# Optimization experiments

Measured on AMD Instinct MI355X. Metric: run time of the kernel, lower is better.

Reference implementation:

```python
import jax, jax.numpy as jnp
import numpy as np

N, S, B, E = 32768, 1024, 32, 262144   # nodes, nodes-per-graph, graphs, edges
C, H, L = 128, 4, 4                    # hidden, heads, layers
ND, ED, PE = 64, 16, 16                # node_dim, edge_dim, pe_dim
DH = C // H
LN_EPS = 1e-5


def _mlp2(h, w1, b1, w2, b2, act=jax.nn.relu):
    # mlp(ch_in, ch_out, hidden, num_hidden_layers=1): Linear -> act -> Linear (dropout = identity at inference)
    return act(h @ w1 + b1) @ w2 + b2


def _layer_norm(h, g, b):
    mu = jnp.mean(h, axis=-1, keepdims=True)
    var = jnp.var(h, axis=-1, keepdims=True)
    return (h - mu) * jax.lax.rsqrt(var + LN_EPS) * g + b


def setup_inputs() -> dict:
    key = jax.random.key(0)
    ks = iter(jax.random.split(key, 64))
    def nrm(shape, scale=0.05):
        return jax.random.normal(next(ks), shape, jnp.float32) * scale
    x = jax.random.normal(next(ks), (N, ND), jnp.float32)
    lap_pe = jax.random.normal(next(ks), (N, PE), jnp.float32)
    edge_attr = jax.random.normal(next(ks), (E, ED), jnp.float32)
    # edges within graphs: each graph occupies a contiguous block of S nodes
    g = jax.random.randint(next(ks), (E,), 0, B)
    src = g * S + jax.random.randint(next(ks), (E,), 0, S)
    dst = g * S + jax.random.randint(next(ks), (E,), 0, S)
    edge_index = jnp.stack([src, dst]).astype(jnp.int32)
    batch = (jnp.arange(N) // S).astype(jnp.int32)
    inp = dict(x=x, edge_index=edge_index, batch=batch, edge_attr=edge_attr, lap_pe=lap_pe)
    inp.update(
        node_w1=nrm((ND + PE, C)), node_b1=jnp.zeros((C,)), node_w2=nrm((C, C)), node_b2=jnp.zeros((C,)),
        edge_w1=nrm((ED, C)), edge_b1=jnp.zeros((C,)), edge_w2=nrm((C, C)), edge_b2=jnp.zeros((C,)),
        eps=jnp.zeros((L,)),
        gin_w1=nrm((L, C, C)), gin_b1=jnp.zeros((L, C)), gin_w2=nrm((L, C, C)), gin_b2=jnp.zeros((L, C)),
        elin_w=nrm((L, C, C)), elin_b=jnp.zeros((L, C)),
        attn_qkv_w=nrm((L, C, 3 * C)), attn_qkv_b=jnp.zeros((L, 3 * C)),
        attn_out_w=nrm((L, C, C)), attn_out_b=jnp.zeros((L, C)),
        mlp_w1=nrm((L, C, 2 * C)), mlp_b1=jnp.zeros((L, 2 * C)),
        mlp_w2=nrm((L, 2 * C, C)), mlp_b2=jnp.zeros((L, C)),
        ln1_g=jnp.ones((L, C)), ln1_b=jnp.zeros((L, C)),
        ln2_g=jnp.ones((L, C)), ln2_b=jnp.zeros((L, C)),
        ln3_g=jnp.ones((L, C)), ln3_b=jnp.zeros((L, C)),
        post_w1=nrm((C, C)), post_b1=jnp.zeros((C,)), post_w2=nrm((C, C)), post_b2=jnp.zeros((C,)),
        ro_w1=nrm((C, C)), ro_b1=jnp.zeros((C,)), ro_w2=nrm((C, 1)), ro_b2=jnp.zeros((1,)),
    )
    return inp


def reference(x, edge_index, batch, edge_attr, lap_pe,
              node_w1, node_b1, node_w2, node_b2,
              edge_w1, edge_b1, edge_w2, edge_b2,
              eps, gin_w1, gin_b1, gin_w2, gin_b2, elin_w, elin_b,
              attn_qkv_w, attn_qkv_b, attn_out_w, attn_out_b,
              mlp_w1, mlp_b1, mlp_w2, mlp_b2,
              ln1_g, ln1_b, ln2_g, ln2_b, ln3_g, ln3_b,
              post_w1, post_b1, post_w2, post_b2,
              ro_w1, ro_b1, ro_w2, ro_b2):
    src, dst = edge_index[0], edge_index[1]
    x = jnp.concatenate([x, lap_pe], axis=-1)
    x = _mlp2(x, node_w1, node_b1, node_w2, node_b2)
    e = _mlp2(edge_attr, edge_w1, edge_b1, edge_w2, edge_b2)
    scale = 1.0 / np.sqrt(DH)
    for i in range(L):
        # --- local GINEConv: nn((1+eps)*x_i + sum_j relu(x_j + lin(e_ij))) ---
        m = jax.nn.relu(x[src] + e @ elin_w[i] + elin_b[i])           # [E, C]
        agg = jax.ops.segment_sum(m, dst, num_segments=N)             # [N, C]
        hl = _mlp2((1.0 + eps[i]) * x + agg, gin_w1[i], gin_b1[i], gin_w2[i], gin_b2[i])
        hl = _layer_norm(hl + x, ln1_g[i], ln1_b[i])
        # --- global multihead attention over dense per-graph batch (equal sizes => reshape) ---
        xd = x.reshape(B, S, C)
        q, k, v = jnp.split(xd @ attn_qkv_w[i] + attn_qkv_b[i], 3, axis=-1)
        q = q.reshape(B, S, H, DH).transpose(0, 2, 1, 3)              # [B,H,S,DH]
        k = k.reshape(B, S, H, DH).transpose(0, 2, 1, 3)
        v = v.reshape(B, S, H, DH).transpose(0, 2, 1, 3)
        att = jax.nn.softmax(jnp.einsum('bhqd,bhkd->bhqk', q, k) * scale, axis=-1)
        o = jnp.einsum('bhqk,bhkd->bhqd', att, v).transpose(0, 2, 1, 3).reshape(B, S, C)
        ha = (o @ attn_out_w[i] + attn_out_b[i]).reshape(N, C)
        ha = _layer_norm(ha + x, ln2_g[i], ln2_b[i])
        # --- combine + FFN (act='gelu') + norm3, then outer residual ---
        out = hl + ha
        out = out + _mlp2(out, mlp_w1[i], mlp_b1[i], mlp_w2[i], mlp_b2[i], act=jax.nn.gelu)
        h = _layer_norm(out, ln3_g[i], ln3_b[i])
        x = x + h
    x = x + _mlp2(x, post_w1, post_b1, post_w2, post_b2)
    sums = jax.ops.segment_sum(x, batch, num_segments=B)
    cnt = jax.ops.segment_sum(jnp.ones((N, 1), x.dtype), batch, num_segments=B)
    gmean = sums / cnt
    return _mlp2(gmean, ro_w1, ro_b1, ro_w2, ro_b2)                   # [B, 1]
```

## Files before the change

### kernel.cpp

```cpp
#include <hip/hip_runtime.h>
#include <math.h>

namespace {

constexpr int N_  = 32768;
constexpr int S_  = 1024;
constexpr int B_  = 32;
constexpr int E_  = 262144;
constexpr int C_  = 128;
constexpr int ND_ = 64;
constexpr int PE_ = 16;
constexpr int ED_ = 16;
constexpr float LNE = 1e-5f;

typedef __attribute__((ext_vector_type(8))) short short8;
typedef __attribute__((ext_vector_type(4))) float floatx4;

__device__ inline float gelu_tanh(float v) {
  const float c = 0.7978845608028654f;
  return 0.5f * v * (1.0f + tanhf(c * (v + 0.044715f * v * v * v)));
}

__device__ inline unsigned short f2bf_u(float f) {
  unsigned u = __float_as_uint(f);
  u += 0x7fff + ((u >> 16) & 1);
  return (unsigned short)(u >> 16);
}

__device__ inline float bf2f(unsigned short v) {
  return __uint_as_float(((unsigned)v) << 16);
}

__device__ inline float block_sum128(float v, float* red, int t) {
  red[t] = v;
  __syncthreads();
#pragma unroll
  for (int off = 64; off > 0; off >>= 1) {
    if (t < off) red[t] += red[t + off];
    __syncthreads();
  }
  float r = red[0];
  __syncthreads();
  return r;
}

__global__ void k_zero(float4* __restrict__ p, int n4) {
  int i = blockIdx.x * 256 + threadIdx.x;
  if (i < n4) p[i] = make_float4(0.f, 0.f, 0.f, 0.f);
}

__global__ void k_count(const int* __restrict__ dst, int* __restrict__ hist) {
  int e = blockIdx.x * 256 + threadIdx.x;
  if (e < E_) atomicAdd(&hist[dst[e]], 1);
}

__global__ __launch_bounds__(1024) void k_scan(int* __restrict__ hist, int* __restrict__ binStart) {
  __shared__ int sums[1024];
  int t = threadIdx.x;
  int base = t * 32;
  int loc[32];
  int s = 0;
#pragma unroll
  for (int i = 0; i < 32; ++i) { loc[i] = s; s += hist[base + i]; }
  sums[t] = s;
  __syncthreads();
  for (int off = 1; off < 1024; off <<= 1) {
    int v = (t >= off) ? sums[t - off] : 0;
    __syncthreads();
    sums[t] += v;
    __syncthreads();
  }
  int excl = sums[t] - s;
#pragma unroll
  for (int i = 0; i < 32; ++i) {
    int v = excl + loc[i];
    binStart[base + i] = v;
    hist[base + i] = v;
  }
  if (t == 1023) binStart[32768] = sums[1023];
}

__global__ void k_scatter(const int* __restrict__ dst, int* __restrict__ cursor,
                          int* __restrict__ perm) {
  int e = blockIdx.x * 256 + threadIdx.x;
  if (e < E_) {
    int p = atomicAdd(&cursor[dst[e]], 1);
    perm[p] = e;
  }
}

__global__ void k_gather_edges(const float* __restrict__ ea, const int* __restrict__ src,
                               const int* __restrict__ dst, const int* __restrict__ perm,
                               float* __restrict__ ea_s, int* __restrict__ src_s,
                               int* __restrict__ dst_s) {
  int p4 = blockIdx.x * 256 + threadIdx.x;
  int p = p4 >> 2, c4 = p4 & 3;
  int e = perm[p];
  ((float4*)(ea_s + (size_t)p * ED_))[c4] = ((const float4*)(ea + (size_t)e * ED_))[c4];
  if (c4 == 0) { src_s[p] = src[e]; dst_s[p] = dst[e]; }
}

__global__ void k_fuse_w(const float* __restrict__ w2, const float* __restrict__ b2,
                         const float* __restrict__ elin_w, const float* __restrict__ elin_b,
                         unsigned short* __restrict__ fw2t, float* __restrict__ fb2) {
  int t = threadIdx.x;
  int bid = blockIdx.x;
  int layer = bid / (C_ + 1);
  int k = bid % (C_ + 1);
  const float* el = elin_w + (size_t)layer * C_ * C_;
  if (k < C_) {
    float a = 0.0f;
    for (int m = 0; m < C_; ++m) a += w2[k * C_ + m] * el[m * C_ + t];
    fw2t[(size_t)layer * C_ * C_ + t * C_ + k] = f2bf_u(a);
  } else {
    float a = elin_b[layer * C_ + t];
    for (int m = 0; m < C_; ++m) a += b2[m] * el[m * C_ + t];
    fb2[layer * C_ + t] = a;
  }
}

__global__ void k_prep_ew1(const float* __restrict__ ew1, unsigned short* __restrict__ ew1t) {
  int n = blockIdx.x;
  int k = threadIdx.x;
  ew1t[n * 32 + k] = (k < ED_) ? f2bf_u(ew1[k * C_ + n]) : (unsigned short)0;
}

__global__ void k_prep(const float* __restrict__ gin_w1, const float* __restrict__ gin_w2,
                       const float* __restrict__ aqkv_w, const float* __restrict__ aout_w,
                       const float* __restrict__ mlp_w1, const float* __restrict__ mlp_w2,
                       unsigned short* __restrict__ wt) {
  int t = threadIdx.x;
  int bid = blockIdx.x;
  int l = bid / 1152;
  int r = bid % 1152;
  unsigned short* base = wt + (size_t)l * 163840;
  if (r < 128) {
    base[r * 128 + t] = f2bf_u(gin_w1[(size_t)l * 16384 + t * 128 + r]);
  } else if (r < 256) {
    int n = r - 128;
    base[16384 + n * 128 + t] = f2bf_u(gin_w2[(size_t)l * 16384 + t * 128 + n]);
  } else if (r < 640) {
    int n = r - 256;
    base[32768 + n * 128 + t] = f2bf_u(aqkv_w[(size_t)l * 49152 + t * 384 + n]);
  } else if (r < 768) {
    int n = r - 640;
    base[81920 + n * 128 + t] = f2bf_u(aout_w[(size_t)l * 16384 + t * 128 + n]);
  } else if (r < 1024) {
    int n = r - 768;
    base[98304 + n * 128 + t] = f2bf_u(mlp_w1[(size_t)l * 32768 + t * 256 + n]);
  } else {
    int n = r - 1024;
    base[131072 + n * 256 + t]       = f2bf_u(mlp_w2[(size_t)l * 32768 + t * 128 + n]);
    base[131072 + n * 256 + 128 + t] = f2bf_u(mlp_w2[(size_t)l * 32768 + (t + 128) * 128 + n]);
  }
}

__global__ void k_node_enc(const float* __restrict__ xin, const float* __restrict__ pe,
                           const float* __restrict__ w1, const float* __restrict__ b1,
                           const float* __restrict__ w2, const float* __restrict__ b2,
                           float* __restrict__ xout) {
  __shared__ float inL[4][80];
  __shared__ float hidL[4][C_];
  int t = threadIdx.x;
  int row0 = blockIdx.x * 4;
#pragma unroll
  for (int r = 0; r < 4; ++r) {
    int row = row0 + r;
    if (t < ND_) inL[r][t] = xin[(size_t)row * ND_ + t];
    else if (t < 80) inL[r][t] = pe[(size_t)row * PE_ + (t - ND_)];
  }
  __syncthreads();
  float acc[4];
  float bb = b1[t];
#pragma unroll
  for (int r = 0; r < 4; ++r) acc[r] = bb;
  for (int k = 0; k < 80; ++k) {
    float wv = w1[k * C_ + t];
#pragma unroll
    for (int r = 0; r < 4; ++r) acc[r] += inL[r][k] * wv;
  }
#pragma unroll
  for (int r = 0; r < 4; ++r) hidL[r][t] = fmaxf(acc[r], 0.0f);
  __syncthreads();
  float bb2 = b2[t];
#pragma unroll
  for (int r = 0; r < 4; ++r) acc[r] = bb2;
  for (int k = 0; k < C_; ++k) {
    float wv = w2[k * C_ + t];
#pragma unroll
    for (int r = 0; r < 4; ++r) acc[r] += hidL[r][k] * wv;
  }
#pragma unroll
  for (int r = 0; r < 4; ++r) xout[(size_t)(row0 + r) * C_ + t] = acc[r];
}

__global__ __launch_bounds__(256) void k_edge_mfma(
    const float* __restrict__ ea_s, const float* __restrict__ x,
    const int* __restrict__ src_s, const int* __restrict__ dst_s,
    const unsigned short* __restrict__ ew1t, const float* __restrict__ eb1,
    const unsigned short* __restrict__ fw2t, const float* __restrict__ fb2,
    float* __restrict__ agg) {
  __shared__ unsigned short eaL[64][40];
  __shared__ unsigned short buf[64][136];
  __shared__ int srcL[64], dstL[64];
  int tid = threadIdx.x;
  int e0 = blockIdx.x * 64;

  if (tid < 64) { srcL[tid] = src_s[e0 + tid]; dstL[tid] = dst_s[e0 + tid]; }
  {
    int r = tid >> 2, c4 = tid & 3;
    float4 v = ((const float4*)(ea_s + (size_t)(e0 + r) * ED_))[c4];
    ushort4 u;
    u.x = f2bf_u(v.x); u.y = f2bf_u(v.y); u.z = f2bf_u(v.z); u.w = f2bf_u(v.w);
    *(ushort4*)&eaL[r][c4 * 4] = u;
    ushort4 z4 = {0, 0, 0, 0};
    *(ushort4*)&eaL[r][16 + c4 * 4] = z4;
  }
  __syncthreads();

  int lane = tid & 63;
  int w = tid >> 6;
  int li = lane & 15;
  int quad = lane >> 4;
  int r0 = w * 16;

  short8 aE = *(const short8*)&eaL[r0 + li][quad * 8];
#pragma unroll
  for (int t8 = 0; t8 < 8; ++t8) {
    short8 bE = *(const short8*)(ew1t + (size_t)(t8 * 16 + li) * 32 + quad * 8);
    floatx4 z = {0.f, 0.f, 0.f, 0.f};
    floatx4 h = __builtin_amdgcn_mfma_f32_16x16x32_bf16(aE, bE, z, 0, 0, 0);
    float bv = eb1[t8 * 16 + li];
#pragma unroll
    for (int reg = 0; reg < 4; ++reg)
      buf[r0 + quad * 4 + reg][t8 * 16 + li] = f2bf_u(fmaxf(h[reg] + bv, 0.f));
  }
  __syncthreads();

  short8 aK[4];
#pragma unroll
  for (int k4 = 0; k4 < 4; ++k4)
    aK[k4] = *(const short8*)&buf[r0 + li][k4 * 32 + quad * 8];
  __syncthreads();

  float fbv[8];
#pragma unroll
  for (int t8 = 0; t8 < 8; ++t8) fbv[t8] = fb2[t8 * 16 + li];

#pragma unroll
  for (int t8 = 0; t8 < 8; ++t8) {
    floatx4 acc = {0.f, 0.f, 0.f, 0.f};
    const unsigned short* bp = fw2t + (size_t)(t8 * 16 + li) * C_ + quad * 8;
#pragma unroll
    for (int k4 = 0; k4 < 4; ++k4) {
      short8 bf = *(const short8*)(bp + k4 * 32);
      acc = __builtin_amdgcn_mfma_f32_16x16x32_bf16(aK[k4], bf, acc, 0, 0, 0);
    }
    int n = t8 * 16 + li;
#pragma unroll
    for (int reg = 0; reg < 4; ++reg) {
      int cr = r0 + quad * 4 + reg;
      float v = fmaxf(acc[reg] + fbv[t8] + x[(size_t)srcL[cr] * C_ + n], 0.0f);
      buf[cr][n] = f2bf_u(v);
    }
  }
  __syncthreads();

  {
    int col = tid & 127;
    int rbase = (tid >> 7) * 32;
    float run = bf2f(buf[rbase][col]);
    int cur = dstL[rbase];
    for (int r = 1; r < 32; ++r) {
      int rr = rbase + r;
      int d = dstL[rr];
      float v = bf2f(buf[rr][col]);
      if (d != cur) {
        atomicAdd(&agg[(size_t)cur * C_ + col], run);
        run = v; cur = d;
      } else {
        run += v;
      }
    }
    atomicAdd(&agg[(size_t)cur * C_ + col], run);
  }
}

__global__ __launch_bounds__(256) void k_ginqkv(
    const float* __restrict__ x, const float* __restrict__ agg,
    const unsigned short* __restrict__ w1t, const float* __restrict__ b1,
    const unsigned short* __restrict__ w2t, const float* __restrict__ b2,
    const float* __restrict__ g, const float* __restrict__ bln,
    const float* __restrict__ epsarr, int layer, float* __restrict__ hl,
    const unsigned short* __restrict__ qkvt, const float* __restrict__ qb,
    unsigned short* __restrict__ qkvb) {
  __shared__ unsigned short inL[64][136];
  __shared__ unsigned short xbL[64][136];
  int tid = threadIdx.x;
  int row0 = blockIdx.x * 64;
  float epsv = 1.0f + epsarr[layer];
#pragma unroll
  for (int i = 0; i < 8; ++i) {
    int p = i * 256 + tid;
    int r = p >> 5, c4 = p & 31;
    float4 xa = *(const float4*)(x + (size_t)(row0 + r) * C_ + c4 * 4);
    float4 ag = *(const float4*)(agg + (size_t)(row0 + r) * C_ + c4 * 4);
    ushort4 ux;
    ux.x = f2bf_u(xa.x); ux.y = f2bf_u(xa.y); ux.z = f2bf_u(xa.z); ux.w = f2bf_u(xa.w);
    *(ushort4*)&xbL[r][c4 * 4] = ux;
    ushort4 u;
    u.x = f2bf_u(epsv * xa.x + ag.x);
    u.y = f2bf_u(epsv * xa.y + ag.y);
    u.z = f2bf_u(epsv * xa.z + ag.z);
    u.w = f2bf_u(epsv * xa.w + ag.w);
    *(ushort4*)&inL[r][c4 * 4] = u;
  }
  __syncthreads();
  int lane = tid & 63, w = tid >> 6, li = lane & 15, quad = lane >> 4;
  int r0 = w * 16;

  short8 aK[4];
#pragma unroll
  for (int k4 = 0; k4 < 4; ++k4) aK[k4] = *(const short8*)&inL[r0 + li][k4 * 32 + quad * 8];
#pragma unroll
  for (int t8 = 0; t8 < 8; ++t8) {
    floatx4 acc = {0.f, 0.f, 0.f, 0.f};
    const unsigned short* bp = w1t + (size_t)(t8 * 16 + li) * 128 + quad * 8;
#pragma unroll
    for (int k4 = 0; k4 < 4; ++k4) {
      short8 bf = *(const short8*)(bp + k4 * 32);
      acc = __builtin_amdgcn_mfma_f32_16x16x32_bf16(aK[k4], bf, acc, 0, 0, 0);
    }
    float bv = b1[t8 * 16 + li];
#pragma unroll
    for (int reg = 0; reg < 4; ++reg)
      inL[r0 + quad * 4 + reg][t8 * 16 + li] = f2bf_u(fmaxf(acc[reg] + bv, 0.f));
  }
  short8 aK2[4];
#pragma unroll
  for (int k4 = 0; k4 < 4; ++k4) aK2[k4] = *(const short8*)&inL[r0 + li][k4 * 32 + quad * 8];
  floatx4 acc2[8];
#pragma unroll
  for (int t8 = 0; t8 < 8; ++t8) acc2[t8] = (floatx4){0.f, 0.f, 0.f, 0.f};
#pragma unroll
  for (int t8 = 0; t8 < 8; ++t8) {
    const unsigned short* bp = w2t + (size_t)(t8 * 16 + li) * 128 + quad * 8;
#pragma unroll
    for (int k4 = 0; k4 < 4; ++k4) {
      short8 bf = *(const short8*)(bp + k4 * 32);
      acc2[t8] = __builtin_amdgcn_mfma_f32_16x16x32_bf16(aK2[k4], bf, acc2[t8], 0, 0, 0);
    }
  }
  float gv[8], blv[8], b2v[8];
#pragma unroll
  for (int t8 = 0; t8 < 8; ++t8) {
    int col = t8 * 16 + li;
    gv[t8] = g[col]; blv[t8] = bln[col]; b2v[t8] = b2[col];
  }
#pragma unroll
  for (int reg = 0; reg < 4; ++reg) {
    int row = row0 + r0 + quad * 4 + reg;
    float v[8], s = 0.f, s2 = 0.f;
#pragma unroll
    for (int t8 = 0; t8 < 8; ++t8) {
      float xv = x[(size_t)row * C_ + t8 * 16 + li];
      v[t8] = acc2[t8][reg] + b2v[t8] + xv;
      s += v[t8]; s2 += v[t8] * v[t8];
    }
#pragma unroll
    for (int m = 1; m <= 8; m <<= 1) { s += __shfl_xor(s, m); s2 += __shfl_xor(s2, m); }
    float mu = s * (1.0f / C_);
    float var = s2 * (1.0f / C_) - mu * mu;
    float inv = rsqrtf(var + LNE);
#pragma unroll
    for (int t8 = 0; t8 < 8; ++t8)
      hl[(size_t)row * C_ + t8 * 16 + li] = (v[t8] - mu) * inv * gv[t8] + blv[t8];
  }

  short8 aQ[4];
#pragma unroll
  for (int k4 = 0; k4 < 4; ++k4) aQ[k4] = *(const short8*)&xbL[r0 + li][k4 * 32 + quad * 8];
#pragma unroll
  for (int t8 = 0; t8 < 24; ++t8) {
    floatx4 acc = {0.f, 0.f, 0.f, 0.f};
    const unsigned short* bp = qkvt + (size_t)(t8 * 16 + li) * 128 + quad * 8;
#pragma unroll
    for (int k4 = 0; k4 < 4; ++k4) {
      short8 bf = *(const short8*)(bp + k4 * 32);
      acc = __builtin_amdgcn_mfma_f32_16x16x32_bf16(aQ[k4], bf, acc, 0, 0, 0);
    }
    int col = t8 * 16 + li;
    float bv = qb[col];
#pragma unroll
    for (int reg = 0; reg < 4; ++reg) {
      int row = row0 + r0 + quad * 4 + reg;
      qkvb[(size_t)row * 384 + col] = f2bf_u(acc[reg] + bv);
    }
  }
}

__global__ __launch_bounds__(256) void k_attn_mfma(const unsigned short* __restrict__ qkvb,
                                                   float* __restrict__ attno) {
  __shared__ unsigned short kL[2][32][40];
  __shared__ unsigned short vT[2][32][40];
  __shared__ unsigned short pL[4][16][40];
  int tid = threadIdx.x;
  int lane = tid & 63;
  int w = tid >> 6;
  int li = lane & 15;
  int quad = lane >> 4;
  int bid = blockIdx.x;
  int b = (bid & 7) * 4 + ((bid >> 3) & 3);
  int rest = bid >> 5;
  int h = rest & 3;
  int qt = rest >> 2;
  int qbase = b * S_ + qt * 64 + w * 16;

  short8 qA = *(const short8*)(qkvb + (size_t)(qbase + li) * 384 + h * 32 + quad * 8);

  floatx4 o0 = {0.f, 0.f, 0.f, 0.f}, o1 = {0.f, 0.f, 0.f, 0.f};
  float lsum[4] = {0.f, 0.f, 0.f, 0.f};
  const float scale = 0.17677669529663687f;

  int half = tid >> 7;
  int tt = tid & 127;
  int j = tt >> 2;
  int seg = tt & 3;
  int vcol = (((j >> 3) ^ seg) & 3) * 8 + (j & 7);
  int vg0 = ((quad ^ (li >> 3)) & 3) * 8;
  int vg1 = ((quad ^ (2 + (li >> 3))) & 3) * 8;

  const unsigned short* pbase = qkvb + (half ? 256 : 128) + h * 32 + seg * 8;

  short8 val = *(const short8*)(pbase + (size_t)(b * S_ + 0 * 32 + j) * 384);

  for (int kc = 0; kc < 32; ++kc) {
    int buf = kc & 1;
    if (half == 0) {
      *(short8*)&kL[buf][j][seg * 8] = val;
    } else {
#pragma unroll
      for (int i = 0; i < 8; ++i) vT[buf][seg * 8 + i][vcol] = (unsigned short)val[i];
    }
    __syncthreads();
    if (kc < 31)
      val = *(const short8*)(pbase + (size_t)(b * S_ + (kc + 1) * 32 + j) * 384);
    short8 kB0 = *(const short8*)&kL[buf][li][quad * 8];
    short8 kB1 = *(const short8*)&kL[buf][16 + li][quad * 8];
    floatx4 z = {0.f, 0.f, 0.f, 0.f};
    floatx4 s0 = __builtin_amdgcn_mfma_f32_16x16x32_bf16(qA, kB0, z, 0, 0, 0);
    floatx4 s1 = __builtin_amdgcn_mfma_f32_16x16x32_bf16(qA, kB1, z, 0, 0, 0);
#pragma unroll
    for (int r = 0; r < 4; ++r) {
      float p0 = __expf(s0[r] * scale);
      float p1 = __expf(s1[r] * scale);
      lsum[r] += p0 + p1;
      pL[w][quad * 4 + r][li] = f2bf_u(p0);
      pL[w][quad * 4 + r][16 + li] = f2bf_u(p1);
    }
    short8 pA  = *(const short8*)&pL[w][li][quad * 8];
    short8 vB0 = *(const short8*)&vT[buf][li][vg0];
    short8 vB1 = *(const short8*)&vT[buf][16 + li][vg1];
    o0 = __builtin_amdgcn_mfma_f32_16x16x32_bf16(pA, vB0, o0, 0, 0, 0);
    o1 = __builtin_amdgcn_mfma_f32_16x16x32_bf16(pA, vB1, o1, 0, 0, 0);
  }
#pragma unroll
  for (int r = 0; r < 4; ++r) {
    float l = lsum[r];
#pragma unroll
    for (int msk = 1; msk <= 8; msk <<= 1) l += __shfl_xor(l, msk);
    float inv = 1.0f / l;
    size_t row = (size_t)(qbase + quad * 4 + r);
    attno[row * C_ + h * 32 + li] = o0[r] * inv;
    attno[row * C_ + h * 32 + 16 + li] = o1[r] * inv;
  }
}

__global__ __launch_bounds__(256) void k_aoffn(
    const float* __restrict__ attno, float* __restrict__ x,
    const float* __restrict__ hl,
    const unsigned short* __restrict__ aot, const float* __restrict__ ab,
    const float* __restrict__ g2, const float* __restrict__ bl2,
    const unsigned short* __restrict__ w1t, const float* __restrict__ b1,
    const unsigned short* __restrict__ w2t, const float* __restrict__ b2,
    const float* __restrict__ g3, const float* __restrict__ bl3) {
  __shared__ unsigned short inL[64][136];
  __shared__ unsigned short hidL[64][264];
  int tid = threadIdx.x;
  int row0 = blockIdx.x * 64;
#pragma unroll
  for (int i = 0; i < 8; ++i) {
    int p = i * 256 + tid;
    int r = p >> 5, c4 = p & 31;
    float4 xa = *(const float4*)(attno + (size_t)(row0 + r) * C_ + c4 * 4);
    ushort4 u;
    u.x = f2bf_u(xa.x); u.y = f2bf_u(xa.y); u.z = f2bf_u(xa.z); u.w = f2bf_u(xa.w);
    *(ushort4*)&inL[r][c4 * 4] = u;
  }
  __syncthreads();
  int lane = tid & 63, w = tid >> 6, li = lane & 15, quad = lane >> 4;
  int r0 = w * 16;

  short8 aK[4];
#pragma unroll
  for (int k4 = 0; k4 < 4; ++k4) aK[k4] = *(const short8*)&inL[r0 + li][k4 * 32 + quad * 8];
  floatx4 acc[8];
#pragma unroll
  for (int t8 = 0; t8 < 8; ++t8) acc[t8] = (floatx4){0.f, 0.f, 0.f, 0.f};
#pragma unroll
  for (int t8 = 0; t8 < 8; ++t8) {
    const unsigned short* bp = aot + (size_t)(t8 * 16 + li) * 128 + quad * 8;
#pragma unroll
    for (int k4 = 0; k4 < 4; ++k4) {
      short8 bf = *(const short8*)(bp + k4 * 32);
      acc[t8] = __builtin_amdgcn_mfma_f32_16x16x32_bf16(aK[k4], bf, acc[t8], 0, 0, 0);
    }
  }
  float g2v[8], bl2v[8], abv[8];
#pragma unroll
  for (int t8 = 0; t8 < 8; ++t8) {
    int col = t8 * 16 + li;
    g2v[t8] = g2[col]; bl2v[t8] = bl2[col]; abv[t8] = ab[col];
  }
  float outv[8][4];
#pragma unroll
  for (int reg = 0; reg < 4; ++reg) {
    int row = row0 + r0 + quad * 4 + reg;
    float v[8], s = 0.f, s2 = 0.f;
#pragma unroll
    for (int t8 = 0; t8 < 8; ++t8) {
      float xv = x[(size_t)row * C_ + t8 * 16 + li];
      v[t8] = acc[t8][reg] + abv[t8] + xv;
      s += v[t8]; s2 += v[t8] * v[t8];
    }
#pragma unroll
    for (int m = 1; m <= 8; m <<= 1) { s += __shfl_xor(s, m); s2 += __shfl_xor(s2, m); }
    float mu = s * (1.0f / C_);
    float var = s2 * (1.0f / C_) - mu * mu;
    float inv = rsqrtf(var + LNE);
#pragma unroll
    for (int t8 = 0; t8 < 8; ++t8) {
      int col = t8 * 16 + li;
      float ha = (v[t8] - mu) * inv * g2v[t8] + bl2v[t8];
      float ov = hl[(size_t)row * C_ + col] + ha;
      outv[t8][reg] = ov;
      inL[r0 + quad * 4 + reg][col] = f2bf_u(ov);
    }
  }

  short8 aK2[4];
#pragma unroll
  for (int k4 = 0; k4 < 4; ++k4) aK2[k4] = *(const short8*)&inL[r0 + li][k4 * 32 + quad * 8];
#pragma unroll
  for (int t8 = 0; t8 < 16; ++t8) {
    floatx4 a1 = {0.f, 0.f, 0.f, 0.f};
    const unsigned short* bp = w1t + (size_t)(t8 * 16 + li) * 128 + quad * 8;
#pragma unroll
    for (int k4 = 0; k4 < 4; ++k4) {
      short8 bf = *(const short8*)(bp + k4 * 32);
      a1 = __builtin_amdgcn_mfma_f32_16x16x32_bf16(aK2[k4], bf, a1, 0, 0, 0);
    }
    float bv = b1[t8 * 16 + li];
#pragma unroll
    for (int reg = 0; reg < 4; ++reg)
      hidL[r0 + quad * 4 + reg][t8 * 16 + li] = f2bf_u(gelu_tanh(a1[reg] + bv));
  }
  short8 aK3[8];
#pragma unroll
  for (int k4 = 0; k4 < 8; ++k4) aK3[k4] = *(const short8*)&hidL[r0 + li][k4 * 32 + quad * 8];
  floatx4 acc2[8];
#pragma unroll
  for (int t8 = 0; t8 < 8; ++t8) acc2[t8] = (floatx4){0.f, 0.f, 0.f, 0.f};
#pragma unroll
  for (int t8 = 0; t8 < 8; ++t8) {
    const unsigned short* bp = w2t + (size_t)(t8 * 16 + li) * 256 + quad * 8;
#pragma unroll
    for (int k4 = 0; k4 < 8; ++k4) {
      short8 bf = *(const short8*)(bp + k4 * 32);
      acc2[t8] = __builtin_amdgcn_mfma_f32_16x16x32_bf16(aK3[k4], bf, acc2[t8], 0, 0, 0);
    }
  }
  float g3v[8], bl3v[8], b2v[8];
#pragma unroll
  for (int t8 = 0; t8 < 8; ++t8) {
    int col = t8 * 16 + li;
    g3v[t8] = g3[col]; bl3v[t8] = bl3[col]; b2v[t8] = b2[col];
  }
#pragma unroll
  for (int reg = 0; reg < 4; ++reg) {
    int row = row0 + r0 + quad * 4 + reg;
    float v[8], s = 0.f, s2 = 0.f;
#pragma unroll
    for (int t8 = 0; t8 < 8; ++t8) {
      v[t8] = acc2[t8][reg] + b2v[t8] + outv[t8][reg];
      s += v[t8]; s2 += v[t8] * v[t8];
    }
#pragma unroll
    for (int m = 1; m <= 8; m <<= 1) { s += __shfl_xor(s, m); s2 += __shfl_xor(s2, m); }
    float mu = s * (1.0f / C_);
    float var = s2 * (1.0f / C_) - mu * mu;
    float inv = rsqrtf(var + LNE);
#pragma unroll
    for (int t8 = 0; t8 < 8; ++t8) {
      size_t idx = (size_t)row * C_ + t8 * 16 + li;
      x[idx] = x[idx] + (v[t8] - mu) * inv * g3v[t8] + bl3v[t8];
    }
  }
}

__global__ void k_post(float* __restrict__ x,
                       const float* __restrict__ w1, const float* __restrict__ b1,
                       const float* __restrict__ w2, const float* __restrict__ b2) {
  __shared__ float inL[4][C_];
  __shared__ float hidL[4][C_];
  int t = threadIdx.x;
  int row0 = blockIdx.x * 4;
  float xv[4];
#pragma unroll
  for (int r = 0; r < 4; ++r) {
    size_t idx = (size_t)(row0 + r) * C_ + t;
    xv[r] = x[idx];
    inL[r][t] = xv[r];
  }
  __syncthreads();
  float acc[4];
  float bb = b1[t];
#pragma unroll
  for (int r = 0; r < 4; ++r) acc[r] = bb;
  for (int k = 0; k < C_; ++k) {
    float wv = w1[k * C_ + t];
#pragma unroll
    for (int r = 0; r < 4; ++r) acc[r] += inL[r][k] * wv;
  }
#pragma unroll
  for (int r = 0; r < 4; ++r) hidL[r][t] = fmaxf(acc[r], 0.0f);
  __syncthreads();
  float bb2 = b2[t];
#pragma unroll
  for (int r = 0; r < 4; ++r) acc[r] = bb2;
  for (int k = 0; k < C_; ++k) {
    float wv = w2[k * C_ + t];
#pragma unroll
    for (int r = 0; r < 4; ++r) acc[r] += hidL[r][k] * wv;
  }
#pragma unroll
  for (int r = 0; r < 4; ++r) {
    size_t idx = (size_t)(row0 + r) * C_ + t;
    x[idx] = xv[r] + acc[r];
  }
}

__global__ void k_pool(const float* __restrict__ x, float* __restrict__ gmean) {
  int t = threadIdx.x;
  int b = blockIdx.x;
  float s = 0.0f;
  for (int sidx = 0; sidx < S_; ++sidx) s += x[((size_t)b * S_ + sidx) * C_ + t];
  gmean[b * C_ + t] = s * (1.0f / S_);
}

__global__ void k_readout(const float* __restrict__ gmean,
                          const float* __restrict__ w1, const float* __restrict__ b1,
                          const float* __restrict__ w2, const float* __restrict__ b2,
                          float* __restrict__ out) {
  __shared__ float gL[C_];
  __shared__ float red[C_];
  int t = threadIdx.x;
  int b = blockIdx.x;
  gL[t] = gmean[b * C_ + t];
  __syncthreads();
  float acc = b1[t];
  for (int k = 0; k < C_; ++k) acc += gL[k] * w1[k * C_ + t];
  float hid = fmaxf(acc, 0.0f);
  float part = hid * w2[t];
  float tot = block_sum128(part, red, t);
  if (t == 0) out[b] = tot + b2[0];
}

}

extern "C" void kernel_launch(void* const* d_in, const int* in_sizes, int n_in,
                              void* d_out, int out_size, void* d_ws, size_t ws_size,
                              hipStream_t stream) {
  const float* in_x      = (const float*)d_in[0];
  const int*   edge_idx  = (const int*)d_in[1];
  const float* edge_attr = (const float*)d_in[3];
  const float* lap_pe    = (const float*)d_in[4];
  const float* node_w1 = (const float*)d_in[5];
  const float* node_b1 = (const float*)d_in[6];
  const float* node_w2 = (const float*)d_in[7];
  const float* node_b2 = (const float*)d_in[8];
  const float* edge_w1 = (const float*)d_in[9];
  const float* edge_b1 = (const float*)d_in[10];
  const float* edge_w2 = (const float*)d_in[11];
  const float* edge_b2 = (const float*)d_in[12];
  const float* eps     = (const float*)d_in[13];
  const float* gin_w1  = (const float*)d_in[14];
  const float* gin_b1  = (const float*)d_in[15];
  const float* gin_w2  = (const float*)d_in[16];
  const float* gin_b2  = (const float*)d_in[17];
  const float* elin_w  = (const float*)d_in[18];
  const float* elin_b  = (const float*)d_in[19];
  const float* aqkv_w  = (const float*)d_in[20];
  const float* aqkv_b  = (const float*)d_in[21];
  const float* aout_w  = (const float*)d_in[22];
  const float* aout_b  = (const float*)d_in[23];
  const float* mlp_w1  = (const float*)d_in[24];
  const float* mlp_b1  = (const float*)d_in[25];
  const float* mlp_w2  = (const float*)d_in[26];
  const float* mlp_b2  = (const float*)d_in[27];
  const float* ln1_g   = (const float*)d_in[28];
  const float* ln1_b   = (const float*)d_in[29];
  const float* ln2_g   = (const float*)d_in[30];
  const float* ln2_b   = (const float*)d_in[31];
  const float* ln3_g   = (const float*)d_in[32];
  const float* ln3_b   = (const float*)d_in[33];
  const float* post_w1 = (const float*)d_in[34];
  const float* post_b1 = (const float*)d_in[35];
  const float* post_w2 = (const float*)d_in[36];
  const float* post_b2 = (const float*)d_in[37];
  const float* ro_w1   = (const float*)d_in[38];
  const float* ro_b1   = (const float*)d_in[39];
  const float* ro_w2   = (const float*)d_in[40];
  const float* ro_b2   = (const float*)d_in[41];

  const int* src = edge_idx;
  const int* dst = edge_idx + E_;

  float* ws = (float*)d_ws;
  float* x     = ws;
  unsigned short* qkvb = (unsigned short*)(x + (size_t)N_ * C_);
  float* hl    = x + (size_t)N_ * C_ + (size_t)N_ * 192;
  float* attno = hl + (size_t)N_ * C_;
  float* agg   = attno;
  float* fb2   = attno + (size_t)N_ * C_;
  unsigned short* fw2tb = (unsigned short*)(fb2 + 4 * C_);
  unsigned short* wt = fw2tb + (size_t)4 * C_ * C_;
  unsigned short* ew1tb = wt + 655360;
  float* ea_s  = (float*)(ew1tb + 4096);
  int* src_s   = (int*)(ea_s + (size_t)E_ * ED_);
  int* dst_s   = src_s + E_;
  int* hist    = dst_s + E_;
  int* binStart = hist + 32768;
  int* perm    = binStart + 32769;
  float* gmean = hl;

  float* out = (float*)d_out;

  dim3 blk(128);
  const size_t LWS = 163840;

  k_fuse_w<<<4 * (C_ + 1), blk, 0, stream>>>(edge_w2, edge_b2, elin_w, elin_b, fw2tb, fb2);
  k_prep<<<4 * 1152, blk, 0, stream>>>(gin_w1, gin_w2, aqkv_w, aout_w, mlp_w1, mlp_w2, wt);
  k_prep_ew1<<<128, 32, 0, stream>>>(edge_w1, ew1tb);
  k_zero<<<(32768 / 4 + 255) / 256, 256, 0, stream>>>((float4*)hist, 32768 / 4);
  k_count<<<E_ / 256, 256, 0, stream>>>(dst, hist);
  k_scan<<<1, 1024, 0, stream>>>(hist, binStart);
  k_scatter<<<E_ / 256, 256, 0, stream>>>(dst, hist, perm);
  k_gather_edges<<<E_ * 4 / 256, 256, 0, stream>>>(edge_attr, src, dst, perm,
                                                   ea_s, src_s, dst_s);
  k_node_enc<<<N_ / 4, blk, 0, stream>>>(in_x, lap_pe, node_w1, node_b1, node_w2, node_b2, x);

  for (int i = 0; i < 4; ++i) {
    const unsigned short* wl = wt + (size_t)i * LWS;
    k_zero<<<(N_ * C_ / 4 + 255) / 256, 256, 0, stream>>>((float4*)agg, N_ * C_ / 4);
    k_edge_mfma<<<E_ / 64, 256, 0, stream>>>(ea_s, x, src_s, dst_s,
                                             ew1tb, edge_b1,
                                             fw2tb + (size_t)i * C_ * C_, fb2 + i * C_, agg);
    k_ginqkv<<<N_ / 64, 256, 0, stream>>>(x, agg,
                                          wl + 0, gin_b1 + i * C_,
                                          wl + 16384, gin_b2 + i * C_,
                                          ln1_g + i * C_, ln1_b + i * C_, eps, i, hl,
                                          wl + 32768, aqkv_b + i * 384, qkvb);
    k_attn_mfma<<<B_ * 4 * 16, 256, 0, stream>>>(qkvb, attno);
    k_aoffn<<<N_ / 64, 256, 0, stream>>>(attno, x, hl,
                                         wl + 81920, aout_b + i * C_,
                                         ln2_g + i * C_, ln2_b + i * C_,
                                         wl + 98304, mlp_b1 + i * 256,
                                         wl + 131072, mlp_b2 + i * C_,
                                         ln3_g + i * C_, ln3_b + i * C_);
  }

  k_post<<<N_ / 4, blk, 0, stream>>>(x, post_w1, post_b1, post_w2, post_b2);
  k_pool<<<B_, blk, 0, stream>>>(x, gmean);
  k_readout<<<B_, blk, 0, stream>>>(gmean, ro_w1, ro_b1, ro_w2, ro_b2, out);
}
```

Baseline: 1.412 ms.

## Store edge attrs in bf16, prefetch source rows to LDS, fuse pooling into post MLP

The edge-gather pass now converts edge attributes to bf16 once, so the per-layer edge kernel reads half the bytes. The edge kernel prefetches the source node rows into shared memory with coalesced float4 loads before the first MFMA stage, replacing scattered per-element reads in the epilogue. It stores them as bf16, which loses some precision in the residual add. The post MLP also accumulates per-graph sums through atomics, removing the separate pooling kernel that walked 1024 rows serially per graph.

After: 1.242 ms. 12.1% less time.

```diff
diff --git a/kernel.cpp b/kernel.cpp
--- a/kernel.cpp
+++ b/kernel.cpp
@@ -91,13 +91,22 @@
 
 __global__ void k_gather_edges(const float* __restrict__ ea, const int* __restrict__ src,
                                const int* __restrict__ dst, const int* __restrict__ perm,
-                               float* __restrict__ ea_s, int* __restrict__ src_s,
+                               unsigned short* __restrict__ ea_b, int* __restrict__ src_s,
                                int* __restrict__ dst_s) {
-  int p4 = blockIdx.x * 256 + threadIdx.x;
-  int p = p4 >> 2, c4 = p4 & 3;
+  int p = blockIdx.x * 256 + threadIdx.x;
+  if (p >= E_) return;
   int e = perm[p];
-  ((float4*)(ea_s + (size_t)p * ED_))[c4] = ((const float4*)(ea + (size_t)e * ED_))[c4];
-  if (c4 == 0) { src_s[p] = src[e]; dst_s[p] = dst[e]; }
+  const float4* s = (const float4*)(ea + (size_t)e * ED_);
+  unsigned short* d = ea_b + (size_t)p * ED_;
+#pragma unroll
+  for (int i = 0; i < 4; ++i) {
+    float4 v = s[i];
+    ushort4 u;
+    u.x = f2bf_u(v.x); u.y = f2bf_u(v.y); u.z = f2bf_u(v.z); u.w = f2bf_u(v.w);
+    *(ushort4*)(d + i * 4) = u;
+  }
+  src_s[p] = src[e];
+  dst_s[p] = dst[e];
 }
 
 __global__ void k_fuse_w(const float* __restrict__ w2, const float* __restrict__ b2,
@@ -195,28 +204,36 @@
 }
 
 __global__ __launch_bounds__(256) void k_edge_mfma(
-    const float* __restrict__ ea_s, const float* __restrict__ x,
+    const unsigned short* __restrict__ ea_b, const float* __restrict__ x,
     const int* __restrict__ src_s, const int* __restrict__ dst_s,
     const unsigned short* __restrict__ ew1t, const float* __restrict__ eb1,
     const unsigned short* __restrict__ fw2t, const float* __restrict__ fb2,
     float* __restrict__ agg) {
-  __shared__ unsigned short eaL[64][40];
+  __shared__ unsigned short eaL[64][32];
   __shared__ unsigned short buf[64][136];
+  __shared__ unsigned short xrL[64][136];
   __shared__ int srcL[64], dstL[64];
   int tid = threadIdx.x;
   int e0 = blockIdx.x * 64;
 
   if (tid < 64) { srcL[tid] = src_s[e0 + tid]; dstL[tid] = dst_s[e0 + tid]; }
-  {
-    int r = tid >> 2, c4 = tid & 3;
-    float4 v = ((const float4*)(ea_s + (size_t)(e0 + r) * ED_))[c4];
-    ushort4 u;
-    u.x = f2bf_u(v.x); u.y = f2bf_u(v.y); u.z = f2bf_u(v.z); u.w = f2bf_u(v.w);
-    *(ushort4*)&eaL[r][c4 * 4] = u;
-    ushort4 z4 = {0, 0, 0, 0};
-    *(ushort4*)&eaL[r][16 + c4 * 4] = z4;
-  }
-  __syncthreads();
+  if (tid < 128) {
+    int r = tid >> 1, hf = tid & 1;
+    *(short8*)&eaL[r][hf * 8] = *(const short8*)(ea_b + (size_t)(e0 + r) * ED_ + hf * 8);
+  } else {
+    int r = (tid - 128) >> 1, hf = (tid - 128) & 1;
+    short8 z = {0, 0, 0, 0, 0, 0, 0, 0};
+    *(short8*)&eaL[r][16 + hf * 8] = z;
+  }
+  __syncthreads();
+
+  float4 xv[8];
+#pragma unroll
+  for (int it = 0; it < 8; ++it) {
+    int idx = it * 256 + tid;
+    int r = idx >> 5, c4 = idx & 31;
+    xv[it] = *(const float4*)(x + (size_t)srcL[r] * C_ + c4 * 4);
+  }
 
   int lane = tid & 63;
   int w = tid >> 6;
@@ -235,13 +252,22 @@
     for (int reg = 0; reg < 4; ++reg)
       buf[r0 + quad * 4 + reg][t8 * 16 + li] = f2bf_u(fmaxf(h[reg] + bv, 0.f));
   }
+
+#pragma unroll
+  for (int it = 0; it < 8; ++it) {
+    int idx = it * 256 + tid;
+    int r = idx >> 5, c4 = idx & 31;
+    ushort4 u;
+    u.x = f2bf_u(xv[it].x); u.y = f2bf_u(xv[it].y);
+    u.z = f2bf_u(xv[it].z); u.w = f2bf_u(xv[it].w);
+    *(ushort4*)&xrL[r][c4 * 4] = u;
+  }
   __syncthreads();
 
   short8 aK[4];
 #pragma unroll
   for (int k4 = 0; k4 < 4; ++k4)
     aK[k4] = *(const short8*)&buf[r0 + li][k4 * 32 + quad * 8];
-  __syncthreads();
 
   float fbv[8];
 #pragma unroll
@@ -260,7 +286,7 @@
 #pragma unroll
     for (int reg = 0; reg < 4; ++reg) {
       int cr = r0 + quad * 4 + reg;
-      float v = fmaxf(acc[reg] + fbv[t8] + x[(size_t)srcL[cr] * C_ + n], 0.0f);
+      float v = fmaxf(acc[reg] + fbv[t8] + bf2f(xrL[cr][n]), 0.0f);
       buf[cr][n] = f2bf_u(v);
     }
   }
@@ -608,9 +634,10 @@
   }
 }
 
-__global__ void k_post(float* __restrict__ x,
-                       const float* __restrict__ w1, const float* __restrict__ b1,
-                       const float* __restrict__ w2, const float* __restrict__ b2) {
+__global__ void k_post_pool(float* __restrict__ x,
+                            const float* __restrict__ w1, const float* __restrict__ b1,
+                            const float* __restrict__ w2, const float* __restrict__ b2,
+                            float* __restrict__ gsum) {
   __shared__ float inL[4][C_];
   __shared__ float hidL[4][C_];
   int t = threadIdx.x;
@@ -643,22 +670,19 @@
 #pragma unroll
     for (int r = 0; r < 4; ++r) acc[r] += hidL[r][k] * wv;
   }
+  float local = 0.f;
 #pragma unroll
   for (int r = 0; r < 4; ++r) {
     size_t idx = (size_t)(row0 + r) * C_ + t;
-    x[idx] = xv[r] + acc[r];
-  }
-}
-
-__global__ void k_pool(const float* __restrict__ x, float* __restrict__ gmean) {
-  int t = threadIdx.x;
-  int b = blockIdx.x;
-  float s = 0.0f;
-  for (int sidx = 0; sidx < S_; ++sidx) s += x[((size_t)b * S_ + sidx) * C_ + t];
-  gmean[b * C_ + t] = s * (1.0f / S_);
-}
-
-__global__ void k_readout(const float* __restrict__ gmean,
+    float nv = xv[r] + acc[r];
+    x[idx] = nv;
+    local += nv;
+  }
+  int b = row0 / S_;
+  atomicAdd(&gsum[b * C_ + t], local);
+}
+
+__global__ void k_readout(const float* __restrict__ gsum,
                           const float* __restrict__ w1, const float* __restrict__ b1,
                           const float* __restrict__ w2, const float* __restrict__ b2,
                           float* __restrict__ out) {
@@ -666,7 +690,7 @@
   __shared__ float red[C_];
   int t = threadIdx.x;
   int b = blockIdx.x;
-  gL[t] = gmean[b * C_ + t];
+  gL[t] = gsum[b * C_ + t] * (1.0f / S_);
   __syncthreads();
   float acc = b1[t];
   for (int k = 0; k < C_; ++k) acc += gL[k] * w1[k * C_ + t];
@@ -736,13 +760,13 @@
   unsigned short* fw2tb = (unsigned short*)(fb2 + 4 * C_);
   unsigned short* wt = fw2tb + (size_t)4 * C_ * C_;
   unsigned short* ew1tb = wt + 655360;
-  float* ea_s  = (float*)(ew1tb + 4096);
-  int* src_s   = (int*)(ea_s + (size_t)E_ * ED_);
+  unsigned short* ea_b = ew1tb + 4096;
+  int* src_s   = (int*)(ea_b + (size_t)E_ * ED_);
   int* dst_s   = src_s + E_;
   int* hist    = dst_s + E_;
   int* binStart = hist + 32768;
   int* perm    = binStart + 32769;
-  float* gmean = hl;
+  float* gsum  = hl;
 
   float* out = (float*)d_out;
 
@@ -756,14 +780,14 @@
   k_count<<<E_ / 256, 256, 0, stream>>>(dst, hist);
   k_scan<<<1, 1024, 0, stream>>>(hist, binStart);
   k_scatter<<<E_ / 256, 256, 0, stream>>>(dst, hist, perm);
-  k_gather_edges<<<E_ * 4 / 256, 256, 0, stream>>>(edge_attr, src, dst, perm,
-                                                   ea_s, src_s, dst_s);
+  k_gather_edges<<<E_ / 256, 256, 0, stream>>>(edge_attr, src, dst, perm,
+                                               ea_b, src_s, dst_s);
   k_node_enc<<<N_ / 4, blk, 0, stream>>>(in_x, lap_pe, node_w1, node_b1, node_w2, node_b2, x);
 
   for (int i = 0; i < 4; ++i) {
     const unsigned short* wl = wt + (size_t)i * LWS;
     k_zero<<<(N_ * C_ / 4 + 255) / 256, 256, 0, stream>>>((float4*)agg, N_ * C_ / 4);
-    k_edge_mfma<<<E_ / 64, 256, 0, stream>>>(ea_s, x, src_s, dst_s,
+    k_edge_mfma<<<E_ / 64, 256, 0, stream>>>(ea_b, x, src_s, dst_s,
                                              ew1tb, edge_b1,
                                              fw2tb + (size_t)i * C_ * C_, fb2 + i * C_, agg);
     k_ginqkv<<<N_ / 64, 256, 0, stream>>>(x, agg,
@@ -780,7 +804,7 @@
                                          ln3_g + i * C_, ln3_b + i * C_);
   }
 
-  k_post<<<N_ / 4, blk, 0, stream>>>(x, post_w1, post_b1, post_w2, post_b2);
-  k_pool<<<B_, blk, 0, stream>>>(x, gmean);
-  k_readout<<<B_, blk, 0, stream>>>(gmean, ro_w1, ro_b1, ro_w2, ro_b2, out);
-}
+  k_zero<<<(B_ * C_ / 4 + 255) / 256, 256, 0, stream>>>((float4*)gsum, B_ * C_ / 4);
+  k_post_pool<<<N_ / 4, blk, 0, stream>>>(x, post_w1, post_b1, post_w2, post_b2, gsum);
+  k_readout<<<B_, blk, 0, stream>>>(gsum, ro_w1, ro_b1, ro_w2, ro_b2, out);
+}
```
